# Optimization experiments

Measured on AMD Instinct MI355X. Metric: run time of the kernel, lower is better.

The kernel has to match this reference:

```python
import jax, jax.numpy as jnp
import numpy as np
import math

N, S, E, BS = 8, 8192, 256, 8


def setup_inputs() -> dict:
    key = jax.random.key(0)
    k1, k2, k3 = jax.random.split(key, 3)
    seq_vector = jax.random.normal(k1, (N, S, E), dtype=jnp.float32)
    # Conv1d weight [target_dim, source_dim] (kernel size 1 squeezed), default torch init scale
    bound = 1.0 / math.sqrt(E)
    W = jax.random.uniform(k2, (E, E), minval=-bound, maxval=bound, dtype=jnp.float32)
    sigma = math.sqrt(1.0 / (BS * E))
    bias = jax.random.uniform(k3, (BS,), minval=-sigma, maxval=sigma, dtype=jnp.float32)
    return {"seq_vector": seq_vector, "W": W, "bias": bias}


def reference(seq_vector, W, bias):
    n, s, e = seq_vector.shape
    bs = bias.shape[0]
    # 1x1 conv == per-token projection: [N,S,E] x [T,E] -> [N,S,T]
    features = jnp.einsum('nse,te->nst', seq_vector, W)
    # group sequence into blocks: [N, S//bs, bs, T]
    fb = features.reshape(n, s // bs, bs, -1)
    # blockwise causal (strictly lower-triangular) sum == exclusive cumsum over block dim
    excl = jnp.cumsum(fb, axis=2) - fb
    # position i gets bias[i]; position 0 additionally gets bias[0] a second time
    b_eff = bias.at[0].add(bias[0])  # [bs]
    out = excl + b_eff[None, None, :, None]
    return out.reshape(n, s, -1)
```

## Files before the change

### kernel.cpp

```cpp
#include <hip/hip_runtime.h>


typedef short short8 __attribute__((ext_vector_type(8)));
typedef float floatx4 __attribute__((ext_vector_type(4)));
typedef unsigned short ushort4v __attribute__((ext_vector_type(4)));

typedef const __attribute__((address_space(1))) unsigned int* gas_u32p;
typedef __attribute__((address_space(3))) unsigned int* las_u32p;

#define WAIT_VMCNT(n) __builtin_amdgcn_s_waitcnt(0x0F70 | ((n) & 0xF) | ((((n) >> 4) & 0x3) << 14))

__device__ __forceinline__ void gl2lds16(const float* g, float* l) {
    __builtin_amdgcn_global_load_lds((gas_u32p)(const void*)g, (las_u32p)(void*)l, 16, 0, 0);
}

__device__ __forceinline__ unsigned short f2bf(float f) {
    union { float f; unsigned int u; } v;
    v.f = f;
    unsigned int u = v.u + 0x7fffu + ((v.u >> 16) & 1u);
    return (unsigned short)(u >> 16);
}

__device__ __forceinline__ short8 pack8(float4 f0, float4 f1) {
    short8 r;
    r[0] = (short)f2bf(f0.x); r[1] = (short)f2bf(f0.y);
    r[2] = (short)f2bf(f0.z); r[3] = (short)f2bf(f0.w);
    r[4] = (short)f2bf(f1.x); r[5] = (short)f2bf(f1.y);
    r[6] = (short)f2bf(f1.z); r[7] = (short)f2bf(f1.w);
    return r;
}

__global__ __launch_bounds__(256) void wconv_kernel(
    const float* __restrict__ W, unsigned short* __restrict__ Wb)
{
    const int i = (blockIdx.x * 256 + threadIdx.x) * 4;
    float4 f = *(const float4*)(W + i);
    ushort4v v;
    v[0] = f2bf(f.x); v[1] = f2bf(f.y); v[2] = f2bf(f.z); v[3] = f2bf(f.w);
    *(ushort4v*)(Wb + i) = v;
}

__global__ __launch_bounds__(256) void bcl_gemm_kernel(
    const float* __restrict__ X, const unsigned short* __restrict__ Wb,
    const float* __restrict__ bias, float* __restrict__ out)
{
    __shared__ float buf[3][128 * 32];

    const int tid  = threadIdx.x;
    const int lane = tid & 63;
    const int w    = tid >> 6;
    const int bx   = blockIdx.x;
    const int mg   = bx >> 1;
    const int ng   = bx & 1;

    const int cl = lane & 15;
    const int q  = lane >> 4;

    const int srow = lane >> 3;
    const int sseg = (lane & 7) ^ srow;
    const float* gsrc0 = X + (size_t)(mg * 128 + w * 32 + srow) * 256 + sseg * 4;

#define STAGE(c, b)                                                            \
    do {                                                                       \
        const float* _g = gsrc0 + (c) * 32;                                    \
        _Pragma("unroll")                                                      \
        for (int _j = 0; _j < 4; ++_j)                                         \
            gl2lds16(_g + _j * 8 * 256, &buf[b][(w * 32 + _j * 8) * 32]);      \
    } while (0)

    const unsigned short* bBase = Wb + (size_t)(ng * 128 + cl) * 256 + q * 8;

    floatx4 acc[2][8];
    #pragma unroll
    for (int mt = 0; mt < 2; ++mt)
        #pragma unroll
        for (int nt = 0; nt < 8; ++nt)
            acc[mt][nt] = (floatx4){0.f, 0.f, 0.f, 0.f};

    STAGE(0, 0);
    STAGE(1, 1);

    #pragma unroll
    for (int c = 0; c < 8; ++c) {
        WAIT_VMCNT(4);
        __builtin_amdgcn_sched_barrier(0);

        short8 Bf[8];
        #pragma unroll
        for (int nt = 0; nt < 8; ++nt)
            Bf[nt] = *(const short8*)(bBase + nt * 16 * 256 + c * 32);

        float4 af[2][2];
        #pragma unroll
        for (int mt = 0; mt < 2; ++mt)
            #pragma unroll
            for (int h = 0; h < 2; ++h)
                af[mt][h] = *(const float4*)
                    &buf[c % 3][(w * 32 + mt * 16 + cl) * 32 +
                                ((((q << 1) | h) ^ (cl & 7)) << 2)];

        if (c + 2 < 8) STAGE(c + 2, (c + 2) % 3);

        short8 a[2];
        a[0] = pack8(af[0][0], af[0][1]);
        a[1] = pack8(af[1][0], af[1][1]);

        #pragma unroll
        for (int mt = 0; mt < 2; ++mt)
            #pragma unroll
            for (int nt = 0; nt < 8; ++nt)
                acc[mt][nt] = __builtin_amdgcn_mfma_f32_16x16x32_bf16(
                    a[mt], Bf[nt], acc[mt][nt], 0, 0, 0);
    }

    float be[4];
    {
        const int off = (q & 1) * 4;
        be[0] = bias[off + 0];
        be[1] = bias[off + 1];
        be[2] = bias[off + 2];
        be[3] = bias[off + 3];
        if (off == 0) be[0] += bias[0];
    }

    float* epi = &buf[0][w * 32 * 32];

    #pragma unroll
    for (int p = 0; p < 4; ++p) {
        const int mt = p >> 1;
        const bool act = ((q >> 1) == (p & 1));
        #pragma unroll
        for (int nt = 0; nt < 8; ++nt) {
            floatx4 v = acc[mt][nt];
            float p1 = v[0];
            float p2 = p1 + v[1];
            float p3 = p2 + v[2];
            float tot = p3 + v[3];
            float below = __shfl_up(tot, 16);
            float p0 = 0.f;
            if (q & 1) { p0 = below; p1 += below; p2 += below; p3 += below; }
            if (act) {
                float* dst = epi + (q & 1) * 4 * 128 + nt * 16 + cl;
                dst[0]   = p0 + be[0];
                dst[128] = p1 + be[1];
                dst[256] = p2 + be[2];
                dst[384] = p3 + be[3];
            }
        }
        #pragma unroll
        for (int k = 0; k < 4; ++k) {
            const int r   = k * 2 + (lane >> 5);
            const int c32 = lane & 31;
            floatx4 vv = *(const floatx4*)&epi[r * 128 + c32 * 4];
            const size_t grow = (size_t)(mg * 128 + w * 32 + p * 8 + r);
            *(floatx4*)&out[grow * 256 + ng * 128 + c32 * 4] = vv;
        }
    }
#undef STAGE
}

extern "C" void kernel_launch(void* const* d_in, const int* in_sizes, int n_in,
                              void* d_out, int out_size, void* d_ws, size_t ws_size,
                              hipStream_t stream)
{
    const float* X = (const float*)d_in[0];
    const float* W = (const float*)d_in[1];
    const float* B = (const float*)d_in[2];
    float* out = (float*)d_out;
    unsigned short* Wb = (unsigned short*)d_ws;

    wconv_kernel<<<dim3(64), dim3(256), 0, stream>>>(W, Wb);
    bcl_gemm_kernel<<<dim3(1024), dim3(256), 0, stream>>>(X, Wb, B, out);
}
```

Before: 144.6 us.

## Double-buffer W fragments in registers and issue loads before waiting

Prefetches the next K-step's bf16 W fragments into a second register buffer and issues the next X stage to LDS before waiting on the current one, with vmcnt thresholds tuned per step. The intent is to hide global load latency for both operands behind the MFMA work. It also adds a launch_bounds occupancy hint of 3 blocks per CU. The hint may constrain registers, and the extra Bf buffer raises register pressure, which risks spills.

```diff
diff --git a/kernel.cpp b/kernel.cpp
--- a/kernel.cpp
+++ b/kernel.cpp
@@ -40,7 +40,7 @@
     *(ushort4v*)(Wb + i) = v;
 }
 
-__global__ __launch_bounds__(256) void bcl_gemm_kernel(
+__global__ __launch_bounds__(256, 3) void bcl_gemm_kernel(
     const float* __restrict__ X, const unsigned short* __restrict__ Wb,
     const float* __restrict__ bias, float* __restrict__ out)
 {
@@ -77,41 +77,54 @@
         for (int nt = 0; nt < 8; ++nt)
             acc[mt][nt] = (floatx4){0.f, 0.f, 0.f, 0.f};
 
+    short8 Bf[2][8];
+
     STAGE(0, 0);
+    #pragma unroll
+    for (int nt = 0; nt < 8; ++nt)
+        Bf[0][nt] = *(const short8*)(bBase + nt * 16 * 256);
     STAGE(1, 1);
 
-    #pragma unroll
-    for (int c = 0; c < 8; ++c) {
-        WAIT_VMCNT(4);
-        __builtin_amdgcn_sched_barrier(0);
+#define KSTEP(c, ALLOW)                                                        \
+    do {                                                                       \
+        if ((c) + 1 < 8) {                                                     \
+            _Pragma("unroll")                                                  \
+            for (int nt = 0; nt < 8; ++nt)                                     \
+                Bf[((c) + 1) & 1][nt] = *(const short8*)                       \
+                    (bBase + nt * 16 * 256 + ((c) + 1) * 32);                  \
+        }                                                                      \
+        if ((c) + 2 < 8) STAGE((c) + 2, ((c) + 2) % 3);                        \
+        __builtin_amdgcn_sched_barrier(0);                                     \
+        WAIT_VMCNT(ALLOW);                                                     \
+        __builtin_amdgcn_sched_barrier(0);                                     \
+        float4 af[2][2];                                                       \
+        _Pragma("unroll")                                                      \
+        for (int mt = 0; mt < 2; ++mt)                                         \
+            _Pragma("unroll")                                                  \
+            for (int h = 0; h < 2; ++h)                                        \
+                af[mt][h] = *(const float4*)                                   \
+                    &buf[(c) % 3][(w * 32 + mt * 16 + cl) * 32 +               \
+                                  ((((q << 1) | h) ^ (cl & 7)) << 2)];         \
+        short8 a0 = pack8(af[0][0], af[0][1]);                                 \
+        short8 a1 = pack8(af[1][0], af[1][1]);                                 \
+        _Pragma("unroll")                                                      \
+        for (int nt = 0; nt < 8; ++nt) {                                       \
+            acc[0][nt] = __builtin_amdgcn_mfma_f32_16x16x32_bf16(              \
+                a0, Bf[(c) & 1][nt], acc[0][nt], 0, 0, 0);                     \
+            acc[1][nt] = __builtin_amdgcn_mfma_f32_16x16x32_bf16(              \
+                a1, Bf[(c) & 1][nt], acc[1][nt], 0, 0, 0);                     \
+        }                                                                      \
+    } while (0)
 
-        short8 Bf[8];
-        #pragma unroll
-        for (int nt = 0; nt < 8; ++nt)
-            Bf[nt] = *(const short8*)(bBase + nt * 16 * 256 + c * 32);
-
-        float4 af[2][2];
-        #pragma unroll
-        for (int mt = 0; mt < 2; ++mt)
-            #pragma unroll
-            for (int h = 0; h < 2; ++h)
-                af[mt][h] = *(const float4*)
-                    &buf[c % 3][(w * 32 + mt * 16 + cl) * 32 +
-                                ((((q << 1) | h) ^ (cl & 7)) << 2)];
-
-        if (c + 2 < 8) STAGE(c + 2, (c + 2) % 3);
-
-        short8 a[2];
-        a[0] = pack8(af[0][0], af[0][1]);
-        a[1] = pack8(af[1][0], af[1][1]);
-
-        #pragma unroll
-        for (int mt = 0; mt < 2; ++mt)
-            #pragma unroll
-            for (int nt = 0; nt < 8; ++nt)
-                acc[mt][nt] = __builtin_amdgcn_mfma_f32_16x16x32_bf16(
-                    a[mt], Bf[nt], acc[mt][nt], 0, 0, 0);
-    }
+    KSTEP(0, 24);
+    KSTEP(1, 24);
+    KSTEP(2, 24);
+    KSTEP(3, 24);
+    KSTEP(4, 24);
+    KSTEP(5, 24);
+    KSTEP(6, 20);
+    KSTEP(7, 8);
+#undef KSTEP
 
     float be[4];
     {
```

Result: slower. 170.6 us (+18.0%).

## Keep W fragments in registers and stream 32-row X tiles through LDS

Applied to the files above, without the earlier changes.

W is converted once into an MFMA-fragment-friendly layout, and each wave keeps its slice of W (two 16-column tiles across the full K) resident in registers. Each 512-thread block then loops over four 32-row X tiles. The tiles are loaded with register prefetch, converted to bf16 while being written into double-buffered LDS, and run through MFMAs over all of K per tile. Output goes through a swizzled LDS epilogue so full 1 KB rows are stored coalesced. This drops the repeated global reads of W per K chunk and the two-block N split. In exchange it uses more registers and adds block-wide barriers and synchronous global loads in place of async LDS DMA.

```diff
diff --git a/kernel.cpp b/kernel.cpp
--- a/kernel.cpp
+++ b/kernel.cpp
@@ -2,17 +2,9 @@
 
 
 typedef short short8 __attribute__((ext_vector_type(8)));
+typedef short short4v __attribute__((ext_vector_type(4)));
 typedef float floatx4 __attribute__((ext_vector_type(4)));
 typedef unsigned short ushort4v __attribute__((ext_vector_type(4)));
-
-typedef const __attribute__((address_space(1))) unsigned int* gas_u32p;
-typedef __attribute__((address_space(3))) unsigned int* las_u32p;
-
-#define WAIT_VMCNT(n) __builtin_amdgcn_s_waitcnt(0x0F70 | ((n) & 0xF) | ((((n) >> 4) & 0x3) << 14))
-
-__device__ __forceinline__ void gl2lds16(const float* g, float* l) {
-    __builtin_amdgcn_global_load_lds((gas_u32p)(const void*)g, (las_u32p)(void*)l, 16, 0, 0);
-}
 
 __device__ __forceinline__ unsigned short f2bf(float f) {
     union { float f; unsigned int u; } v;
@@ -21,12 +13,10 @@
     return (unsigned short)(u >> 16);
 }
 
-__device__ __forceinline__ short8 pack8(float4 f0, float4 f1) {
-    short8 r;
-    r[0] = (short)f2bf(f0.x); r[1] = (short)f2bf(f0.y);
-    r[2] = (short)f2bf(f0.z); r[3] = (short)f2bf(f0.w);
-    r[4] = (short)f2bf(f1.x); r[5] = (short)f2bf(f1.y);
-    r[6] = (short)f2bf(f1.z); r[7] = (short)f2bf(f1.w);
+__device__ __forceinline__ short4v pack4(float4 f) {
+    short4v r;
+    r[0] = (short)f2bf(f.x); r[1] = (short)f2bf(f.y);
+    r[2] = (short)f2bf(f.z); r[3] = (short)f2bf(f.w);
     return r;
 }
 
@@ -35,83 +25,74 @@
 {
     const int i = (blockIdx.x * 256 + threadIdx.x) * 4;
     float4 f = *(const float4*)(W + i);
+    const int n = i >> 8, k = i & 255;
+    const int idx =
+        (((n >> 4) * 8 + (k >> 5)) * 64 + (n & 15) * 4 + ((k >> 3) & 3)) * 8 +
+        (k & 7);
     ushort4v v;
     v[0] = f2bf(f.x); v[1] = f2bf(f.y); v[2] = f2bf(f.z); v[3] = f2bf(f.w);
-    *(ushort4v*)(Wb + i) = v;
+    *(ushort4v*)(Wb + idx) = v;
 }
 
-__global__ __launch_bounds__(256) void bcl_gemm_kernel(
+__global__ __launch_bounds__(512, 4) void bcl_gemm_kernel(
     const float* __restrict__ X, const unsigned short* __restrict__ Wb,
     const float* __restrict__ bias, float* __restrict__ out)
 {
-    __shared__ float buf[3][128 * 32];
+    __shared__ unsigned short aT[2][32 * 256];
+    __shared__ float epi[32 * 256];
 
     const int tid  = threadIdx.x;
     const int lane = tid & 63;
     const int w    = tid >> 6;
-    const int bx   = blockIdx.x;
-    const int mg   = bx >> 1;
-    const int ng   = bx & 1;
+    const int cl   = lane & 15;
+    const int q    = lane >> 4;
 
-    const int cl = lane & 15;
-    const int q  = lane >> 4;
+    short8 Bf[2][8];
+    #pragma unroll
+    for (int nt = 0; nt < 2; ++nt)
+        #pragma unroll
+        for (int kc = 0; kc < 8; ++kc)
+            Bf[nt][kc] = *(const short8*)
+                (Wb + ((((w * 2 + nt) * 8 + kc) * 64) + cl * 4 + q) * 8);
 
-    const int srow = lane >> 3;
-    const int sseg = (lane & 7) ^ srow;
-    const float* gsrc0 = X + (size_t)(mg * 128 + w * 32 + srow) * 256 + sseg * 4;
+    const int tile0 = blockIdx.x * 4;
+    float4 sF[4];
 
-#define STAGE(c, b)                                                            \
-    do {                                                                       \
-        const float* _g = gsrc0 + (c) * 32;                                    \
-        _Pragma("unroll")                                                      \
-        for (int _j = 0; _j < 4; ++_j)                                         \
-            gl2lds16(_g + _j * 8 * 256, &buf[b][(w * 32 + _j * 8) * 32]);      \
+#define LOADT(tt)                                                             \
+    do {                                                                      \
+        const float* _g = X + (size_t)(tt) * 8192 + tid * 4;                  \
+        _Pragma("unroll")                                                     \
+        for (int _j = 0; _j < 4; ++_j)                                        \
+            sF[_j] = *(const float4*)(_g + _j * 2048);                        \
     } while (0)
 
-    const unsigned short* bBase = Wb + (size_t)(ng * 128 + cl) * 256 + q * 8;
+#define WRITET(b)                                                             \
+    do {                                                                      \
+        _Pragma("unroll")                                                     \
+        for (int _j = 0; _j < 4; ++_j) {                                      \
+            const int _row = _j * 8 + w;                                      \
+            const int _ph  = (lane >> 1) ^ w;                 \
+            *(short4v*)&aT[b][_row * 256 + _ph * 8 + (lane & 1) * 4] =        \
+                pack4(sF[_j]);                                                \
+        }                                                                     \
+    } while (0)
 
-    floatx4 acc[2][8];
-    #pragma unroll
-    for (int mt = 0; mt < 2; ++mt)
-        #pragma unroll
-        for (int nt = 0; nt < 8; ++nt)
-            acc[mt][nt] = (floatx4){0.f, 0.f, 0.f, 0.f};
-
-    STAGE(0, 0);
-    STAGE(1, 1);
-
-    #pragma unroll
-    for (int c = 0; c < 8; ++c) {
-        WAIT_VMCNT(4);
-        __builtin_amdgcn_sched_barrier(0);
-
-        short8 Bf[8];
-        #pragma unroll
-        for (int nt = 0; nt < 8; ++nt)
-            Bf[nt] = *(const short8*)(bBase + nt * 16 * 256 + c * 32);
-
-        float4 af[2][2];
-        #pragma unroll
-        for (int mt = 0; mt < 2; ++mt)
-            #pragma unroll
-            for (int h = 0; h < 2; ++h)
-                af[mt][h] = *(const float4*)
-                    &buf[c % 3][(w * 32 + mt * 16 + cl) * 32 +
-                                ((((q << 1) | h) ^ (cl & 7)) << 2)];
-
-        if (c + 2 < 8) STAGE(c + 2, (c + 2) % 3);
-
-        short8 a[2];
-        a[0] = pack8(af[0][0], af[0][1]);
-        a[1] = pack8(af[1][0], af[1][1]);
-
-        #pragma unroll
-        for (int mt = 0; mt < 2; ++mt)
-            #pragma unroll
-            for (int nt = 0; nt < 8; ++nt)
-                acc[mt][nt] = __builtin_amdgcn_mfma_f32_16x16x32_bf16(
-                    a[mt], Bf[nt], acc[mt][nt], 0, 0, 0);
-    }
+#define COMPUTE(b)                                                            \
+    do {                                                                      \
+        _Pragma("unroll")                                                     \
+        for (int kc = 0; kc < 8; ++kc) {                                      \
+            _Pragma("unroll")                                                 \
+            for (int mt = 0; mt < 2; ++mt) {                                  \
+                short8 _a = *(const short8*)                                  \
+                    &aT[b][(mt * 16 + cl) * 256 +                             \
+                           (((kc * 4 + q) ^ (cl & 7)) << 3)];                 \
+                acc[mt][0] = __builtin_amdgcn_mfma_f32_16x16x32_bf16(         \
+                    _a, Bf[0][kc], acc[mt][0], 0, 0, 0);                      \
+                acc[mt][1] = __builtin_amdgcn_mfma_f32_16x16x32_bf16(         \
+                    _a, Bf[1][kc], acc[mt][1], 0, 0, 0);                      \
+            }                                                                 \
+        }                                                                     \
+    } while (0)
 
     float be[4];
     {
@@ -123,40 +104,60 @@
         if (off == 0) be[0] += bias[0];
     }
 
-    float* epi = &buf[0][w * 32 * 32];
+    floatx4 acc[2][2];
+
+    LOADT(tile0);
+    WRITET(0);
+    __syncthreads();
 
     #pragma unroll
-    for (int p = 0; p < 4; ++p) {
-        const int mt = p >> 1;
-        const bool act = ((q >> 1) == (p & 1));
+    for (int t = 0; t < 4; ++t) {
+        const int tile = tile0 + t;
+        if (t + 1 < 4) LOADT(tile + 1);
+
         #pragma unroll
-        for (int nt = 0; nt < 8; ++nt) {
-            floatx4 v = acc[mt][nt];
-            float p1 = v[0];
-            float p2 = p1 + v[1];
-            float p3 = p2 + v[2];
-            float tot = p3 + v[3];
-            float below = __shfl_up(tot, 16);
-            float p0 = 0.f;
-            if (q & 1) { p0 = below; p1 += below; p2 += below; p3 += below; }
-            if (act) {
-                float* dst = epi + (q & 1) * 4 * 128 + nt * 16 + cl;
+        for (int mt = 0; mt < 2; ++mt)
+            #pragma unroll
+            for (int nt = 0; nt < 2; ++nt)
+                acc[mt][nt] = (floatx4){0.f, 0.f, 0.f, 0.f};
+
+        COMPUTE(t & 1);
+        if (t + 1 < 4) WRITET((t + 1) & 1);
+
+        #pragma unroll
+        for (int mt = 0; mt < 2; ++mt)
+            #pragma unroll
+            for (int nt = 0; nt < 2; ++nt) {
+                floatx4 v = acc[mt][nt];
+                float p1 = v[0];
+                float p2 = p1 + v[1];
+                float p3 = p2 + v[2];
+                float tot = p3 + v[3];
+                float below = __shfl_up(tot, 16);
+                float p0 = 0.f;
+                if (q & 1) { p0 = below; p1 += below; p2 += below; p3 += below; }
+                const int rbase = mt * 16 + q * 4;
+                const int ph = (w * 8 + nt * 4 + (cl >> 2)) ^ (q << 2);
+                float* dst = &epi[rbase * 256 + ph * 4 + (cl & 3)];
                 dst[0]   = p0 + be[0];
-                dst[128] = p1 + be[1];
-                dst[256] = p2 + be[2];
-                dst[384] = p3 + be[3];
+                dst[256] = p1 + be[1];
+                dst[512] = p2 + be[2];
+                dst[768] = p3 + be[3];
             }
-        }
+        __syncthreads();
+
         #pragma unroll
         for (int k = 0; k < 4; ++k) {
-            const int r   = k * 2 + (lane >> 5);
-            const int c32 = lane & 31;
-            floatx4 vv = *(const floatx4*)&epi[r * 128 + c32 * 4];
-            const size_t grow = (size_t)(mg * 128 + w * 32 + p * 8 + r);
-            *(floatx4*)&out[grow * 256 + ng * 128 + c32 * 4] = vv;
+            const int row = w * 4 + k;
+            floatx4 vv = *(const floatx4*)
+                &epi[row * 256 + ((lane ^ ((w & 3) << 2)) << 2)];
+            *(floatx4*)&out[(size_t)(tile * 32 + row) * 256 + lane * 4] = vv;
         }
+        if (t + 1 < 4) __syncthreads();
     }
-#undef STAGE
+#undef LOADT
+#undef WRITET
+#undef COMPUTE
 }
 
 extern "C" void kernel_launch(void* const* d_in, const int* in_sizes, int n_in,
@@ -170,5 +171,5 @@
     unsigned short* Wb = (unsigned short*)d_ws;
 
     wconv_kernel<<<dim3(64), dim3(256), 0, stream>>>(W, Wb);
-    bcl_gemm_kernel<<<dim3(1024), dim3(256), 0, stream>>>(X, Wb, B, out);
+    bcl_gemm_kernel<<<dim3(512), dim3(512), 0, stream>>>(X, Wb, B, out);
 }
```

After: 123.9 us. 14.3% less time.
